# Optimization experiments

Measured on AMD Instinct MI355X. Metric: run time of the kernel, lower is better.

Reference implementation:

```python
import jax, jax.numpy as jnp
import numpy as np

EPS = 1e-5
CHUNK = 512  # chunk of known points for the running-argmin 1-NN search


def nn_idx(unknown, known):
    """1-NN index of each unknown point into known. unknown (B,n,3), known (B,m,3) -> (B,n) int32."""
    B, n, _ = unknown.shape
    m = known.shape[1]
    u2 = jnp.sum(unknown * unknown, axis=-1)  # (B,n)
    # (num_chunks, B, CHUNK, 3)
    kc = known.reshape(B, m // CHUNK, CHUNK, 3).transpose(1, 0, 2, 3)

    def step(carry, kch):
        best_d, best_i, off = carry
        k2 = jnp.sum(kch * kch, axis=-1)  # (B,CHUNK)
        # squared distances for this chunk: (B,n,CHUNK)
        d = u2[:, :, None] - 2.0 * jnp.einsum('bnd,bcd->bnc', unknown, kch) + k2[:, None, :]
        dmin = jnp.min(d, axis=-1)
        imin = jnp.argmin(d, axis=-1).astype(jnp.int32) + off
        upd = dmin < best_d
        return (jnp.where(upd, dmin, best_d), jnp.where(upd, imin, best_i), off + CHUNK), None

    init = (jnp.full((B, n), jnp.inf, unknown.dtype),
            jnp.zeros((B, n), jnp.int32),
            jnp.int32(0))
    (_, best_i, _), _ = jax.lax.scan(step, init, kc)
    return best_i


def bn_relu(x, gamma, beta):
    """Training-mode BatchNorm over (B, n) per channel followed by ReLU. x: (B,C,n)."""
    mean = jnp.mean(x, axis=(0, 2), keepdims=True)
    var = jnp.mean(jnp.square(x - mean), axis=(0, 2), keepdims=True)  # biased, as torch BN
    y = (x - mean) * jax.lax.rsqrt(var + EPS)
    return jax.nn.relu(y * gamma[None, :, None] + beta[None, :, None])


def setup_inputs() -> dict:
    key = jax.random.key(0)
    ks = jax.random.split(key, 8)
    B, n, m, C1, C2 = 2, 65536, 16384, 128, 256
    mlp = [C2 + C1, 256, 128]
    return {
        'unknown': jax.random.normal(ks[0], (B, n, 3), jnp.float32),
        'known': jax.random.normal(ks[1], (B, m, 3), jnp.float32),
        'unknow_feats': jax.random.normal(ks[2], (B, C1, n), jnp.float32),
        'known_feats': jax.random.normal(ks[3], (B, C2, m), jnp.float32),
        'w1': jax.random.normal(ks[4], (mlp[1], mlp[0]), jnp.float32) * (1.0 / np.sqrt(mlp[0])),
        'gamma1': jnp.ones((mlp[1],), jnp.float32),
        'beta1': jnp.zeros((mlp[1],), jnp.float32),
        'w2': jax.random.normal(ks[5], (mlp[2], mlp[1]), jnp.float32) * (1.0 / np.sqrt(mlp[1])),
        'gamma2': jnp.ones((mlp[2],), jnp.float32),
        'beta2': jnp.zeros((mlp[2],), jnp.float32),
    }


def reference(unknown, known, unknow_feats, known_feats, w1, gamma1, beta1, w2, gamma2, beta2):
    idx = nn_idx(unknown, known)  # (B,n) int32
    # gather: (B,C2,m) indexed along m -> (B,C2,n)
    interpolated = jnp.take_along_axis(known_feats, idx[:, None, :], axis=2)
    new_features = jnp.concatenate([interpolated, unknow_feats], axis=1)  # (B,C1+C2,n)
    h = bn_relu(jnp.einsum('oc,bcn->bon', w1, new_features), gamma1, beta1)
    out = bn_relu(jnp.einsum('oc,bcn->bon', w2, h), gamma2, beta2)
    return out  # (B, mlp[-1], n)
```

## Files before the change

### kernel.cpp

```cpp
#include <hip/hip_runtime.h>

typedef unsigned short u16;
typedef unsigned int u32;
typedef __bf16 bf16x8 __attribute__((ext_vector_type(8)));
typedef _Float16 f16;
typedef _Float16 f16x8 __attribute__((ext_vector_type(8)));
typedef float f32x4 __attribute__((ext_vector_type(4)));
typedef float f32x16 __attribute__((ext_vector_type(16)));

#define B_ 2
#define N_ 65536
#define M_ 16384
#define C1_ 128
#define C2_ 256
#define K1_ 384
#define O1_ 256
#define O2_ 128
#define JT_ 512
#define HT_ (JT_/2)
#define EPS2_ 6.0e-3f
#define TFIN_ 1.25e-4f

__device__ __forceinline__ u16 f2bf(float f) {
    u32 u = __float_as_uint(f);
    u32 r = (u + 0x7FFFu + ((u >> 16) & 1u)) >> 16;
    return (u16)r;
}
__device__ __forceinline__ float bf2f(u16 h) {
    return __uint_as_float(((u32)h) << 16);
}
__device__ __forceinline__ u32 pack2(float lo, float hi) {
    return (u32)f2bf(lo) | ((u32)f2bf(hi) << 16);
}
__device__ __forceinline__ uint4 pack8(float4 a, float4 b) {
    uint4 r;
    r.x = pack2(a.x, a.y); r.y = pack2(a.z, a.w);
    r.z = pack2(b.x, b.y); r.w = pack2(b.z, b.w);
    return r;
}
__device__ __forceinline__ u16 h2u(f16 h) {
    union { f16 h; u16 u; } c; c.h = h; return c.u;
}

__device__ __forceinline__ float mul_rn(float a, float b) {
    float p = __fmul_rn(a, b);
    asm volatile("" : "+v"(p));
    return p;
}
__device__ __forceinline__ float sq3_np(float x, float y, float z) {
    return __fadd_rn(__fadd_rn(mul_rn(x, x), mul_rn(y, y)), mul_rn(z, z));
}
__device__ __forceinline__ float dot3_fma(float a0, float b0, float a1, float b1,
                                          float a2, float b2) {
    return fmaf(a2, b2, fmaf(a1, b1, mul_rn(a0, b0)));
}


__global__ __launch_bounds__(256) void k_prep_u(const float* __restrict__ unk,
                                                u16* __restrict__ Aprep) {
    int g = blockIdx.x * 256 + threadIdx.x;
    const float* up = unk + (size_t)g * 3;
    float tx = -2.f * up[0], ty = -2.f * up[1], tz = -2.f * up[2];
    f16 xh = (f16)tx; f16 xl = (f16)(tx - (float)xh);
    f16 yh = (f16)ty; f16 yl = (f16)(ty - (float)yh);
    f16 zh = (f16)tz; f16 zl = (f16)(tz - (float)zh);
    u16 lo[8] = {h2u(xh), h2u(xh), h2u(xl), h2u(yh), h2u(yh), h2u(yl), h2u(zh), h2u(zh)};
    u16 hi[8] = {h2u(zl), 0x3C00u, 0x3C00u, 0, 0, 0, 0, 0};
    u16* tb = Aprep + ((size_t)(g >> 5)) * 512;
    int r = g & 31;
    *(uint4*)(tb + r * 8) = *(uint4*)lo;
    *(uint4*)(tb + (r + 32) * 8) = *(uint4*)hi;
}

__global__ __launch_bounds__(256) void k_prep_k(const float* __restrict__ kn,
                                                u16* __restrict__ Bprep,
                                                float4* __restrict__ kco) {
    int g = blockIdx.x * 256 + threadIdx.x;
    const float* kp = kn + (size_t)g * 3;
    float x = kp[0], y = kp[1], z = kp[2];
    float qv = sq3_np(x, y, z);
    f16 xh = (f16)x; f16 xl = (f16)(x - (float)xh);
    f16 yh = (f16)y; f16 yl = (f16)(y - (float)yh);
    f16 zh = (f16)z; f16 zl = (f16)(z - (float)zh);
    f16 qh = (f16)qv; f16 ql = (f16)(qv - (float)qh);
    u16 lo[8] = {h2u(xh), h2u(xl), h2u(xh), h2u(yh), h2u(yl), h2u(yh), h2u(zh), h2u(zl)};
    u16 hi[8] = {h2u(zh), h2u(qh), h2u(ql), 0x3C00u, 0x3C00u, 0, 0, 0};
    u16* tb = Bprep + ((size_t)(g >> 5)) * 512;
    int r = g & 31;
    *(uint4*)(tb + r * 8) = *(uint4*)lo;
    *(uint4*)(tb + (r + 32) * 8) = *(uint4*)hi;
    kco[g] = make_float4(x, y, z, qv);
}

__global__ __launch_bounds__(256, 4) void k_nn(
        const u16* __restrict__ Aprep, const u16* __restrict__ Bprep,
        const float* __restrict__ unk, const float4* __restrict__ kco,
        unsigned long long* __restrict__ pc) {
    __shared__ unsigned long long cand[256];
    __shared__ float thrS[256];
    const int t = threadIdx.x;
    const int half = blockIdx.y, b = blockIdx.z;
    const int lane = t & 63, w = t >> 6;
    const int rowbase = blockIdx.x * 256;
    const u16* at = Aprep + (((size_t)(b * N_ + rowbase + w * 64)) >> 5) * 512;
    f16x8 af0 = *(const f16x8*)(at + lane * 8);
    f16x8 af1 = *(const f16x8*)(at + 512 + lane * 8);
    const u16* Bp = Bprep + ((size_t)b * JT_ + (size_t)half * HT_) * 512 + lane * 8;
    cand[t] = ~0ULL;

    const f32x16 zz = {0.f,0.f,0.f,0.f,0.f,0.f,0.f,0.f,0.f,0.f,0.f,0.f,0.f,0.f,0.f,0.f};

    f32x16 rm0, rm1;
#pragma unroll
    for (int r = 0; r < 16; ++r) { rm0[r] = 3.4e38f; rm1[r] = 3.4e38f; }

    f16x8 c0 = *(const f16x8*)Bp;
    f16x8 c1 = *(const f16x8*)(Bp + 512);
    for (int tp = 0; tp < HT_; tp += 2) {
        f16x8 n0 = *(const f16x8*)(Bp + 1024);
        f16x8 n1 = *(const f16x8*)(Bp + 1536);
        Bp += 1024;
        f32x16 a  = __builtin_amdgcn_mfma_f32_32x32x16_f16(af0, c0, zz, 0, 0, 0);
        f32x16 ca = __builtin_amdgcn_mfma_f32_32x32x16_f16(af0, c1, zz, 0, 0, 0);
#pragma unroll
        for (int r = 0; r < 16; ++r)
            rm0[r] = fminf(fminf(rm0[r], a[r]), ca[r]);
        a  = __builtin_amdgcn_mfma_f32_32x32x16_f16(af1, c0, zz, 0, 0, 0);
        ca = __builtin_amdgcn_mfma_f32_32x32x16_f16(af1, c1, zz, 0, 0, 0);
#pragma unroll
        for (int r = 0; r < 16; ++r)
            rm1[r] = fminf(fminf(rm1[r], a[r]), ca[r]);
        c0 = n0; c1 = n1;
    }

#pragma unroll
    for (int r = 0; r < 16; ++r) {
        float v0 = rm0[r], v1 = rm1[r];
        v0 = fminf(v0, __shfl_xor(v0, 1));  v1 = fminf(v1, __shfl_xor(v1, 1));
        v0 = fminf(v0, __shfl_xor(v0, 2));  v1 = fminf(v1, __shfl_xor(v1, 2));
        v0 = fminf(v0, __shfl_xor(v0, 4));  v1 = fminf(v1, __shfl_xor(v1, 4));
        v0 = fminf(v0, __shfl_xor(v0, 8));  v1 = fminf(v1, __shfl_xor(v1, 8));
        v0 = fminf(v0, __shfl_xor(v0, 16)); v1 = fminf(v1, __shfl_xor(v1, 16));
        if ((lane & 31) == 0) {
            int rl = w * 64 + ((lane >> 5) << 2) + (r & 3) + 8 * (r >> 2);
            thrS[rl] = v0 + EPS2_;
            thrS[rl + 32] = v1 + EPS2_;
        }
    }
    if (lane >= 32) {
        float tf0 = thrS[w * 64 + (lane & 31)] + TFIN_;
        f16 h0 = (f16)(-tf0);
        af0[3] = h0; af0[4] = (f16)(-tf0 - (float)h0);
        float tf1 = thrS[w * 64 + 32 + (lane & 31)] + TFIN_;
        f16 h1 = (f16)(-tf1);
        af1[3] = h1; af1[4] = (f16)(-tf1 - (float)h1);
    }

    const float4* kcb = kco + (size_t)b * M_;
    const float* ub = unk + (size_t)b * N_ * 3;
    const int rloc0 = w * 64 + ((lane >> 5) << 2);
    const int jb0 = half * (M_ / 2);

    Bp -= (size_t)HT_ * 512;
    c0 = *(const f16x8*)Bp;
    f16x8 c1b = *(const f16x8*)(Bp + 512);
    for (int tt = 0; tt < HT_; ++tt) {
        f16x8 nx = *(const f16x8*)(Bp + 1024);
        Bp += 512;
        f32x16 a0 = __builtin_amdgcn_mfma_f32_32x32x16_f16(af0, c0, zz, 0, 0, 0);
        f32x16 a1 = __builtin_amdgcn_mfma_f32_32x32x16_f16(af1, c0, zz, 0, 0, 0);
        u32 o = 0;
#pragma unroll
        for (int r = 0; r < 16; ++r)
            o |= __float_as_uint(a0[r]) | __float_as_uint(a1[r]);
        if (__ballot((int)o < 0)) {
            int j = jb0 + tt * 32 + (lane & 31);
            float4 kc = kcb[j];
#pragma unroll
            for (int r = 0; r < 16; ++r) {
                if (a0[r] <= 0.f) {
                    int rl = rloc0 + (r & 3) + 8 * (r >> 2);
                    const float* up = ub + (size_t)(rowbase + rl) * 3;
                    float x = up[0], y = up[1], zc = up[2];
                    float uq = sq3_np(x, y, zc);
                    float dot = dot3_fma(x, kc.x, y, kc.y, zc, kc.z);
                    float d = __fadd_rn(fmaf(-2.0f, dot, uq), kc.w);
                    u32 db = __float_as_uint(d);
                    db = (db & 0x80000000u) ? ~db : (db | 0x80000000u);
                    atomicMin(&cand[rl], ((unsigned long long)db << 32) | (u32)j);
                }
                if (a1[r] <= 0.f) {
                    int rl = rloc0 + 32 + (r & 3) + 8 * (r >> 2);
                    const float* up = ub + (size_t)(rowbase + rl) * 3;
                    float x = up[0], y = up[1], zc = up[2];
                    float uq = sq3_np(x, y, zc);
                    float dot = dot3_fma(x, kc.x, y, kc.y, zc, kc.z);
                    float d = __fadd_rn(fmaf(-2.0f, dot, uq), kc.w);
                    u32 db = __float_as_uint(d);
                    db = (db & 0x80000000u) ? ~db : (db | 0x80000000u);
                    atomicMin(&cand[rl], ((unsigned long long)db << 32) | (u32)j);
                }
            }
        }
        c0 = c1b; c1b = nx;
    }
    pc[((size_t)(half * B_ + b)) * N_ + rowbase + t] = cand[t];
}

__global__ __launch_bounds__(256) void k_nn_merge(
        const unsigned long long* __restrict__ pc, int* __restrict__ idx) {
    int g = blockIdx.x * 256 + threadIdx.x;
    unsigned long long a = pc[g];
    unsigned long long c = pc[(size_t)(B_ * N_) + g];
    idx[g] = (int)(u32)((c < a ? c : a) & 0xFFFFFFFFu);
}

__global__ __launch_bounds__(256) void k_tr_kf(const float* __restrict__ kf,
                                               u16* __restrict__ kfT) {
    __shared__ float lt[64][65];
    const int t = threadIdx.x, b = blockIdx.z;
    const int j0 = blockIdx.x * 64, c0 = blockIdx.y * 64;
    const int jl = t & 63, cl4 = t >> 6;
#pragma unroll
    for (int p = 0; p < 16; ++p) {
        int c = c0 + cl4 + p * 4;
        lt[cl4 + p * 4][jl] = kf[((size_t)(b * C2_ + c)) * M_ + j0 + jl];
    }
    __syncthreads();
    const int cl = t & 63, jr4 = t >> 6;
#pragma unroll
    for (int p = 0; p < 16; ++p) {
        int j = j0 + jr4 + p * 4;
        kfT[((size_t)(b * M_ + j)) * C2_ + c0 + cl] = f2bf(lt[cl][jr4 + p * 4]);
    }
}

__global__ __launch_bounds__(256) void k_tr_uf(const float* __restrict__ uf,
                                               u16* __restrict__ newF) {
    __shared__ float lt[64][65];
    const int t = threadIdx.x, b = blockIdx.z;
    const int i0 = blockIdx.x * 64, c0 = blockIdx.y * 64;
    const int il = t & 63, cl4 = t >> 6;
#pragma unroll
    for (int p = 0; p < 16; ++p) {
        int c = c0 + cl4 + p * 4;
        lt[cl4 + p * 4][il] = uf[((size_t)(b * C1_ + c)) * N_ + i0 + il];
    }
    __syncthreads();
    const int cl = t & 63, ir4 = t >> 6;
#pragma unroll
    for (int p = 0; p < 16; ++p) {
        int i = i0 + ir4 + p * 4;
        newF[((size_t)(b * N_ + i)) * K1_ + C2_ + c0 + cl] = f2bf(lt[cl][ir4 + p * 4]);
    }
}

__global__ __launch_bounds__(256) void k_gather(const u16* __restrict__ kfT,
                                                const int* __restrict__ idx,
                                                u16* __restrict__ newF) {
    const int t = threadIdx.x, b = blockIdx.y;
    const int il = t >> 5, qq = t & 31;
    const int i = blockIdx.x * 8 + il;
    const int j = idx[b * N_ + i];
    const uint4* src = (const uint4*)(kfT + ((size_t)(b * M_ + j)) * C2_) + qq;
    uint4* dst = (uint4*)(newF + ((size_t)(b * N_ + i)) * K1_) + qq;
    *dst = *src;
}

__global__ __launch_bounds__(256) void k_gemm1(const u16* __restrict__ newF,
                                               const float* __restrict__ w1,
                                               u16* __restrict__ y1) {
    __shared__ u16 As[128 * 40];
    __shared__ u16 Bs[128 * 40];
    const int t = threadIdx.x, b = blockIdx.z;
    const int i0 = blockIdx.x * 128, o0 = blockIdx.y * 128;
    const int lane = t & 63, wv = t >> 6, wr = wv >> 1, wc = wv & 1;
    const int col = lane & 15, q = lane >> 4;

    const int rA0 = t >> 2, sA0 = t & 3;
    const u16* aS0 = newF + ((size_t)(b * N_ + i0 + rA0)) * K1_ + sA0 * 8;
    const u16* aS1 = aS0 + (size_t)64 * K1_;
    const float* bS0 = w1 + (size_t)(o0 + rA0) * K1_ + sA0 * 8;
    const float* bS1 = bS0 + (size_t)64 * K1_;
    u16* aD0 = &As[rA0 * 40 + sA0 * 8];
    u16* aD1 = aD0 + 64 * 40;
    u16* bD0 = &Bs[rA0 * 40 + sA0 * 8];
    u16* bD1 = bD0 + 64 * 40;

    f32x4 acc[4][4];
#pragma unroll
    for (int m = 0; m < 4; ++m)
#pragma unroll
        for (int n = 0; n < 4; ++n) acc[m][n] = (f32x4){0.f, 0.f, 0.f, 0.f};

    uint4 a0 = *(const uint4*)aS0, a1 = *(const uint4*)aS1;
    float4 f00 = *(const float4*)bS0, f01 = *(const float4*)(bS0 + 4);
    float4 f10 = *(const float4*)bS1, f11 = *(const float4*)(bS1 + 4);

    for (int ks = 0; ks < 12; ++ks) {
        __syncthreads();
        *(uint4*)aD0 = a0; *(uint4*)aD1 = a1;
        *(uint4*)bD0 = pack8(f00, f01); *(uint4*)bD1 = pack8(f10, f11);
        __syncthreads();
        if (ks < 11) {
            int ko = (ks + 1) * 32;
            a0 = *(const uint4*)(aS0 + ko); a1 = *(const uint4*)(aS1 + ko);
            f00 = *(const float4*)(bS0 + ko); f01 = *(const float4*)(bS0 + ko + 4);
            f10 = *(const float4*)(bS1 + ko); f11 = *(const float4*)(bS1 + ko + 4);
        }
        const u16* ap = &As[(wr * 64 + col) * 40 + q * 8];
        const u16* bp = &Bs[(wc * 64 + col) * 40 + q * 8];
        bf16x8 af[4], bfr[4];
#pragma unroll
        for (int m = 0; m < 4; ++m) af[m] = *(const bf16x8*)(ap + m * 640);
#pragma unroll
        for (int n = 0; n < 4; ++n) bfr[n] = *(const bf16x8*)(bp + n * 640);
#pragma unroll
        for (int m = 0; m < 4; ++m)
#pragma unroll
            for (int n = 0; n < 4; ++n)
                acc[m][n] = __builtin_amdgcn_mfma_f32_16x16x32_bf16(af[m], bfr[n], acc[m][n], 0, 0, 0);
    }
#pragma unroll
    for (int m = 0; m < 4; ++m)
#pragma unroll
        for (int n = 0; n < 4; ++n) {
            int go = o0 + wc * 64 + n * 16 + col;
#pragma unroll
            for (int r = 0; r < 4; ++r) {
                int gi = i0 + wr * 64 + m * 16 + q * 4 + r;
                y1[((size_t)(b * N_ + gi)) * O1_ + go] = f2bf(acc[m][n][r]);
            }
        }
}

__global__ __launch_bounds__(256) void k_stats_bf16(const u16* __restrict__ y1,
                                                    float* __restrict__ sum,
                                                    float* __restrict__ sq) {
    const int t = threadIdx.x;
    const int row0 = blockIdx.x * 1024;
    float s = 0.f, qq = 0.f;
    for (int r = 0; r < 1024; ++r) {
        float v = bf2f(y1[((size_t)(row0 + r)) * O1_ + t]);
        s += v; qq = fmaf(v, v, qq);
    }
    atomicAdd(&sum[t], s);
    atomicAdd(&sq[t], qq);
}

__global__ __launch_bounds__(256) void k_stats_f32(const float* __restrict__ y2,
                                                   float* __restrict__ sum,
                                                   float* __restrict__ sq) {
    const int t = threadIdx.x;
    const int o = t & 127, h = t >> 7;
    const int row0 = blockIdx.x * 1024;
    float s = 0.f, qq = 0.f;
    for (int r = 0; r < 512; ++r) {
        float v = y2[((size_t)(row0 + r * 2 + h)) * O2_ + o];
        s += v; qq = fmaf(v, v, qq);
    }
    atomicAdd(&sum[o], s);
    atomicAdd(&sq[o], qq);
}

__global__ void k_bn_fin(const float* __restrict__ sum, const float* __restrict__ sq,
                         const float* __restrict__ gamma, const float* __restrict__ beta,
                         float* __restrict__ scale, float* __restrict__ bias,
                         int C, float invN) {
    int t = threadIdx.x;
    if (t < C) {
        float mean = sum[t] * invN;
        float var = sq[t] * invN - mean * mean;
        float rs = rsqrtf(var + 1e-5f);
        float sc = gamma[t] * rs;
        scale[t] = sc;
        bias[t] = beta[t] - mean * sc;
    }
}

__global__ __launch_bounds__(256) void k_gemm2(const u16* __restrict__ y1,
                                               const float* __restrict__ w2,
                                               const float* __restrict__ s1,
                                               const float* __restrict__ b1,
                                               float* __restrict__ y2) {
    __shared__ u16 As[128 * 40];
    __shared__ u16 Bs[128 * 40];
    const int t = threadIdx.x, b = blockIdx.z;
    const int i0 = blockIdx.x * 128;
    const int lane = t & 63, wv = t >> 6, wr = wv >> 1, wc = wv & 1;
    const int col = lane & 15, q = lane >> 4;

    const int rA0 = t >> 2, sA0 = t & 3;
    const u16* aS0 = y1 + ((size_t)(b * N_ + i0 + rA0)) * O1_ + sA0 * 8;
    const u16* aS1 = aS0 + (size_t)64 * O1_;
    const float* bS0 = w2 + (size_t)rA0 * O1_ + sA0 * 8;
    const float* bS1 = bS0 + (size_t)64 * O1_;
    u16* aD0 = &As[rA0 * 40 + sA0 * 8];
    u16* aD1 = aD0 + 64 * 40;
    u16* bD0 = &Bs[rA0 * 40 + sA0 * 8];
    u16* bD1 = bD0 + 64 * 40;

    f32x4 acc[4][4];
#pragma unroll
    for (int m = 0; m < 4; ++m)
#pragma unroll
        for (int n = 0; n < 4; ++n) acc[m][n] = (f32x4){0.f, 0.f, 0.f, 0.f};

    uint4 a0 = *(const uint4*)aS0, a1 = *(const uint4*)aS1;
    float4 f00 = *(const float4*)bS0, f01 = *(const float4*)(bS0 + 4);
    float4 f10 = *(const float4*)bS1, f11 = *(const float4*)(bS1 + 4);

    for (int ks = 0; ks < 8; ++ks) {
        int oc = ks * 32 + sA0 * 8;
        float4 sc0 = *(const float4*)(s1 + oc), sc1 = *(const float4*)(s1 + oc + 4);
        float4 bb0 = *(const float4*)(b1 + oc), bb1 = *(const float4*)(b1 + oc + 4);
        uint4 h0, h1;
        {
            const u16* hs = (const u16*)&a0;
            float v[8];
            v[0] = fmaxf(fmaf(bf2f(hs[0]), sc0.x, bb0.x), 0.f);
            v[1] = fmaxf(fmaf(bf2f(hs[1]), sc0.y, bb0.y), 0.f);
            v[2] = fmaxf(fmaf(bf2f(hs[2]), sc0.z, bb0.z), 0.f);
            v[3] = fmaxf(fmaf(bf2f(hs[3]), sc0.w, bb0.w), 0.f);
            v[4] = fmaxf(fmaf(bf2f(hs[4]), sc1.x, bb1.x), 0.f);
            v[5] = fmaxf(fmaf(bf2f(hs[5]), sc1.y, bb1.y), 0.f);
            v[6] = fmaxf(fmaf(bf2f(hs[6]), sc1.z, bb1.z), 0.f);
            v[7] = fmaxf(fmaf(bf2f(hs[7]), sc1.w, bb1.w), 0.f);
            h0.x = pack2(v[0], v[1]); h0.y = pack2(v[2], v[3]);
            h0.z = pack2(v[4], v[5]); h0.w = pack2(v[6], v[7]);
        }
        {
            const u16* hs = (const u16*)&a1;
            float v[8];
            v[0] = fmaxf(fmaf(bf2f(hs[0]), sc0.x, bb0.x), 0.f);
            v[1] = fmaxf(fmaf(bf2f(hs[1]), sc0.y, bb0.y), 0.f);
            v[2] = fmaxf(fmaf(bf2f(hs[2]), sc0.z, bb0.z), 0.f);
            v[3] = fmaxf(fmaf(bf2f(hs[3]), sc0.w, bb0.w), 0.f);
            v[4] = fmaxf(fmaf(bf2f(hs[4]), sc1.x, bb1.x), 0.f);
            v[5] = fmaxf(fmaf(bf2f(hs[5]), sc1.y, bb1.y), 0.f);
            v[6] = fmaxf(fmaf(bf2f(hs[6]), sc1.z, bb1.z), 0.f);
            v[7] = fmaxf(fmaf(bf2f(hs[7]), sc1.w, bb1.w), 0.f);
            h1.x = pack2(v[0], v[1]); h1.y = pack2(v[2], v[3]);
            h1.z = pack2(v[4], v[5]); h1.w = pack2(v[6], v[7]);
        }
        __syncthreads();
        *(uint4*)aD0 = h0; *(uint4*)aD1 = h1;
        *(uint4*)bD0 = pack8(f00, f01); *(uint4*)bD1 = pack8(f10, f11);
        __syncthreads();
        if (ks < 7) {
            int ko = (ks + 1) * 32;
            a0 = *(const uint4*)(aS0 + ko); a1 = *(const uint4*)(aS1 + ko);
            f00 = *(const float4*)(bS0 + ko); f01 = *(const float4*)(bS0 + ko + 4);
            f10 = *(const float4*)(bS1 + ko); f11 = *(const float4*)(bS1 + ko + 4);
        }
        const u16* ap = &As[(wr * 64 + col) * 40 + q * 8];
        const u16* bp = &Bs[(wc * 64 + col) * 40 + q * 8];
        bf16x8 af[4], bfr[4];
#pragma unroll
        for (int m = 0; m < 4; ++m) af[m] = *(const bf16x8*)(ap + m * 640);
#pragma unroll
        for (int n = 0; n < 4; ++n) bfr[n] = *(const bf16x8*)(bp + n * 640);
#pragma unroll
        for (int m = 0; m < 4; ++m)
#pragma unroll
            for (int n = 0; n < 4; ++n)
                acc[m][n] = __builtin_amdgcn_mfma_f32_16x16x32_bf16(af[m], bfr[n], acc[m][n], 0, 0, 0);
    }
#pragma unroll
    for (int m = 0; m < 4; ++m)
#pragma unroll
        for (int n = 0; n < 4; ++n) {
            int go = wc * 64 + n * 16 + col;
#pragma unroll
            for (int r = 0; r < 4; ++r) {
                int gi = i0 + wr * 64 + m * 16 + q * 4 + r;
                y2[((size_t)(b * N_ + gi)) * O2_ + go] = acc[m][n][r];
            }
        }
}

__global__ __launch_bounds__(256) void k_out(const float* __restrict__ y2,
                                             const float* __restrict__ s2,
                                             const float* __restrict__ b2,
                                             float* __restrict__ out) {
    __shared__ float lt[64 * 65];
    const int t = threadIdx.x, b = blockIdx.z;
    const int i0 = blockIdx.x * 64, o0 = blockIdx.y * 64;
    const int oc = t & 63, ir4 = t >> 6;
    const float sc = s2[o0 + oc], bs = b2[o0 + oc];
#pragma unroll
    for (int p = 0; p < 16; ++p) {
        int i = i0 + ir4 + p * 4;
        float v = y2[((size_t)(b * N_ + i)) * O2_ + o0 + oc];
        lt[oc * 65 + ir4 + p * 4] = fmaxf(fmaf(v, sc, bs), 0.f);
    }
    __syncthreads();
    const int il = t & 63, or4 = t >> 6;
#pragma unroll
    for (int p = 0; p < 16; ++p) {
        int o = o0 + or4 + p * 4;
        out[((size_t)(b * O2_ + o)) * N_ + i0 + il] = lt[(or4 + p * 4) * 65 + il];
    }
}

extern "C" void kernel_launch(void* const* d_in, const int* in_sizes, int n_in,
                              void* d_out, int out_size, void* d_ws, size_t ws_size,
                              hipStream_t stream) {
    const float* unknown = (const float*)d_in[0];
    const float* known   = (const float*)d_in[1];
    const float* uf      = (const float*)d_in[2];
    const float* kf      = (const float*)d_in[3];
    const float* w1      = (const float*)d_in[4];
    const float* g1      = (const float*)d_in[5];
    const float* be1     = (const float*)d_in[6];
    const float* w2      = (const float*)d_in[7];
    const float* g2      = (const float*)d_in[8];
    const float* be2     = (const float*)d_in[9];
    float* out = (float*)d_out;

    char* w = (char*)d_ws;
    float* bn1_sum = (float*)w;
    float* bn1_sq  = bn1_sum + 256;
    float* bn2_sum = bn1_sq + 256;
    float* bn2_sq  = bn2_sum + 128;
    float* s1 = (float*)(w + 4096);
    float* b1 = s1 + 256;
    float* s2 = b1 + 256;
    float* b2 = s2 + 128;
    int* idx = (int*)(w + 8192);
    u16* newF = (u16*)(w + 532480);
    float* y2 = (float*)(w + 532480);
    size_t R2 = 532480 + 100663296ULL;
    u16*   Aprep = (u16*)(w + R2);
    u16*   Bprep = (u16*)(w + R2 + 4194304ULL);
    float4* kco  = (float4*)(w + R2 + 5242880ULL);
    unsigned long long* pc = (unsigned long long*)(w + R2 + 5767168ULL);
    u16*  kfT = (u16*)(w + R2 + 16777216ULL);
    u16*   y1 = (u16*)(w + R2);

    hipMemsetAsync(w, 0, 3072, stream);

    k_prep_u<<<512, 256, 0, stream>>>(unknown, Aprep);
    k_prep_k<<<128, 256, 0, stream>>>(known, Bprep, kco);
    k_nn<<<dim3(N_ / 256, 2, B_), 256, 0, stream>>>(Aprep, Bprep, unknown, kco, pc);
    k_nn_merge<<<512, 256, 0, stream>>>(pc, idx);
    k_tr_kf<<<dim3(256, 4, 2), 256, 0, stream>>>(kf, kfT);
    k_tr_uf<<<dim3(1024, 2, 2), 256, 0, stream>>>(uf, newF);
    k_gather<<<dim3(8192, 2), 256, 0, stream>>>(kfT, idx, newF);
    k_gemm1<<<dim3(512, 2, 2), 256, 0, stream>>>(newF, w1, y1);
    k_stats_bf16<<<128, 256, 0, stream>>>(y1, bn1_sum, bn1_sq);
    k_bn_fin<<<1, 256, 0, stream>>>(bn1_sum, bn1_sq, g1, be1, s1, b1, 256, 1.f / 131072.f);
    k_gemm2<<<dim3(512, 1, 2), 256, 0, stream>>>(y1, w2, s1, b1, y2);
    k_stats_f32<<<128, 256, 0, stream>>>(y2, bn2_sum, bn2_sq);
    k_bn_fin<<<1, 256, 0, stream>>>(bn2_sum, bn2_sq, g2, be2, s2, b2, 128, 1.f / 131072.f);
    k_out<<<dim3(1024, 2, 2), 256, 0, stream>>>(y2, s2, b2, out);
}
```

Before: 582.2 us.

## Fuse BN statistics into GEMM epilogues, rescale NN filter, add group-level refine skip

The BatchNorm sum and sum-of-squares reductions move into the epilogues of both GEMM kernels, using wave shuffles and atomics, so the two separate stats kernels and their full re-reads of y1 and y2 are dropped. The fp16 MFMA distance filter in the NN kernel is rescaled by 256 to use more of fp16's range, with the candidate threshold constants scaled to match. The filter-hit test now uses per-group mins with __any, so refinement runs only for row groups that actually have candidates. Risks: atomic float accumulation order changes the BN statistics slightly, and the rescaled fp16 thresholds could change which candidates pass the filter.

```diff
diff --git a/kernel.cpp b/kernel.cpp
--- a/kernel.cpp
+++ b/kernel.cpp
@@ -18,8 +18,8 @@
 #define O2_ 128
 #define JT_ 512
 #define HT_ (JT_/2)
-#define EPS2_ 6.0e-3f
-#define TFIN_ 1.25e-4f
+#define EPS2_ 131.072f
+#define TFIN_ 8.0f
 
 __device__ __forceinline__ u16 f2bf(float f) {
     u32 u = __float_as_uint(f);
@@ -60,12 +60,12 @@
                                                 u16* __restrict__ Aprep) {
     int g = blockIdx.x * 256 + threadIdx.x;
     const float* up = unk + (size_t)g * 3;
-    float tx = -2.f * up[0], ty = -2.f * up[1], tz = -2.f * up[2];
+    float tx = -512.f * up[0], ty = -512.f * up[1], tz = -512.f * up[2];
     f16 xh = (f16)tx; f16 xl = (f16)(tx - (float)xh);
     f16 yh = (f16)ty; f16 yl = (f16)(ty - (float)yh);
     f16 zh = (f16)tz; f16 zl = (f16)(tz - (float)zh);
     u16 lo[8] = {h2u(xh), h2u(xh), h2u(xl), h2u(yh), h2u(yh), h2u(yl), h2u(zh), h2u(zh)};
-    u16 hi[8] = {h2u(zl), 0x3C00u, 0x3C00u, 0, 0, 0, 0, 0};
+    u16 hi[8] = {h2u(zl), 0x5C00u, 0x5C00u, 0, 0, 0, 0, 0};
     u16* tb = Aprep + ((size_t)(g >> 5)) * 512;
     int r = g & 31;
     *(uint4*)(tb + r * 8) = *(uint4*)lo;
@@ -79,12 +79,13 @@
     const float* kp = kn + (size_t)g * 3;
     float x = kp[0], y = kp[1], z = kp[2];
     float qv = sq3_np(x, y, z);
-    f16 xh = (f16)x; f16 xl = (f16)(x - (float)xh);
-    f16 yh = (f16)y; f16 yl = (f16)(y - (float)yh);
-    f16 zh = (f16)z; f16 zl = (f16)(z - (float)zh);
-    f16 qh = (f16)qv; f16 ql = (f16)(qv - (float)qh);
+    float sx = 256.f * x, sy = 256.f * y, sz = 256.f * z, sq = 256.f * qv;
+    f16 xh = (f16)sx; f16 xl = (f16)(sx - (float)xh);
+    f16 yh = (f16)sy; f16 yl = (f16)(sy - (float)yh);
+    f16 zh = (f16)sz; f16 zl = (f16)(sz - (float)zh);
+    f16 qh = (f16)sq; f16 ql = (f16)(sq - (float)qh);
     u16 lo[8] = {h2u(xh), h2u(xl), h2u(xh), h2u(yh), h2u(yl), h2u(yh), h2u(zh), h2u(zl)};
-    u16 hi[8] = {h2u(zh), h2u(qh), h2u(ql), 0x3C00u, 0x3C00u, 0, 0, 0};
+    u16 hi[8] = {h2u(zh), h2u(qh), h2u(ql), 0x5C00u, 0x5C00u, 0, 0, 0};
     u16* tb = Bprep + ((size_t)(g >> 5)) * 512;
     int r = g & 31;
     *(uint4*)(tb + r * 8) = *(uint4*)lo;
@@ -148,10 +149,10 @@
         }
     }
     if (lane >= 32) {
-        float tf0 = thrS[w * 64 + (lane & 31)] + TFIN_;
+        float tf0 = (thrS[w * 64 + (lane & 31)] + TFIN_) * 0.00390625f;
         f16 h0 = (f16)(-tf0);
         af0[3] = h0; af0[4] = (f16)(-tf0 - (float)h0);
-        float tf1 = thrS[w * 64 + 32 + (lane & 31)] + TFIN_;
+        float tf1 = (thrS[w * 64 + 32 + (lane & 31)] + TFIN_) * 0.00390625f;
         f16 h1 = (f16)(-tf1);
         af1[3] = h1; af1[4] = (f16)(-tf1 - (float)h1);
     }
@@ -160,6 +161,19 @@
     const float* ub = unk + (size_t)b * N_ * 3;
     const int rloc0 = w * 64 + ((lane >> 5) << 2);
     const int jb0 = half * (M_ / 2);
+
+#define REFINE(RL, AV)                                                         \
+    if ((AV) <= 0.f) {                                                         \
+        int rl = (RL);                                                         \
+        const float* up = ub + (size_t)(rowbase + rl) * 3;                     \
+        float x = up[0], y = up[1], zc = up[2];                                \
+        float uq = sq3_np(x, y, zc);                                           \
+        float dot = dot3_fma(x, kc.x, y, kc.y, zc, kc.z);                      \
+        float d = __fadd_rn(fmaf(-2.0f, dot, uq), kc.w);                       \
+        u32 db = __float_as_uint(d);                                           \
+        db = (db & 0x80000000u) ? ~db : (db | 0x80000000u);                    \
+        atomicMin(&cand[rl], ((unsigned long long)db << 32) | (u32)j);         \
+    }
 
     Bp -= (size_t)HT_ * 512;
     c0 = *(const f16x8*)Bp;
@@ -169,41 +183,34 @@
         Bp += 512;
         f32x16 a0 = __builtin_amdgcn_mfma_f32_32x32x16_f16(af0, c0, zz, 0, 0, 0);
         f32x16 a1 = __builtin_amdgcn_mfma_f32_32x32x16_f16(af1, c0, zz, 0, 0, 0);
-        u32 o = 0;
-#pragma unroll
-        for (int r = 0; r < 16; ++r)
-            o |= __float_as_uint(a0[r]) | __float_as_uint(a1[r]);
-        if (__ballot((int)o < 0)) {
+        float gm0[4], gm1[4];
+#pragma unroll
+        for (int g = 0; g < 4; ++g) {
+            gm0[g] = fminf(fminf(a0[4*g], a0[4*g+1]), fminf(a0[4*g+2], a0[4*g+3]));
+            gm1[g] = fminf(fminf(a1[4*g], a1[4*g+1]), fminf(a1[4*g+2], a1[4*g+3]));
+        }
+        float gall = fminf(fminf(fminf(gm0[0], gm0[1]), fminf(gm0[2], gm0[3])),
+                           fminf(fminf(gm1[0], gm1[1]), fminf(gm1[2], gm1[3])));
+        if (__ballot(gall <= 0.f)) {
             int j = jb0 + tt * 32 + (lane & 31);
             float4 kc = kcb[j];
 #pragma unroll
-            for (int r = 0; r < 16; ++r) {
-                if (a0[r] <= 0.f) {
-                    int rl = rloc0 + (r & 3) + 8 * (r >> 2);
-                    const float* up = ub + (size_t)(rowbase + rl) * 3;
-                    float x = up[0], y = up[1], zc = up[2];
-                    float uq = sq3_np(x, y, zc);
-                    float dot = dot3_fma(x, kc.x, y, kc.y, zc, kc.z);
-                    float d = __fadd_rn(fmaf(-2.0f, dot, uq), kc.w);
-                    u32 db = __float_as_uint(d);
-                    db = (db & 0x80000000u) ? ~db : (db | 0x80000000u);
-                    atomicMin(&cand[rl], ((unsigned long long)db << 32) | (u32)j);
+            for (int g = 0; g < 4; ++g) {
+                if (__any(gm0[g] <= 0.f)) {
+#pragma unroll
+                    for (int rr = 0; rr < 4; ++rr)
+                        REFINE(rloc0 + 8 * g + rr, a0[4*g+rr])
                 }
-                if (a1[r] <= 0.f) {
-                    int rl = rloc0 + 32 + (r & 3) + 8 * (r >> 2);
-                    const float* up = ub + (size_t)(rowbase + rl) * 3;
-                    float x = up[0], y = up[1], zc = up[2];
-                    float uq = sq3_np(x, y, zc);
-                    float dot = dot3_fma(x, kc.x, y, kc.y, zc, kc.z);
-                    float d = __fadd_rn(fmaf(-2.0f, dot, uq), kc.w);
-                    u32 db = __float_as_uint(d);
-                    db = (db & 0x80000000u) ? ~db : (db | 0x80000000u);
-                    atomicMin(&cand[rl], ((unsigned long long)db << 32) | (u32)j);
+                if (__any(gm1[g] <= 0.f)) {
+#pragma unroll
+                    for (int rr = 0; rr < 4; ++rr)
+                        REFINE(rloc0 + 32 + 8 * g + rr, a1[4*g+rr])
                 }
             }
         }
         c0 = c1b; c1b = nx;
     }
+#undef REFINE
     pc[((size_t)(half * B_ + b)) * N_ + rowbase + t] = cand[t];
 }
 
@@ -269,7 +276,9 @@
 
 __global__ __launch_bounds__(256) void k_gemm1(const u16* __restrict__ newF,
                                                const float* __restrict__ w1,
-                                               u16* __restrict__ y1) {
+                                               u16* __restrict__ y1,
+                                               float* __restrict__ bsum,
+                                               float* __restrict__ bsq) {
     __shared__ u16 As[128 * 40];
     __shared__ u16 Bs[128 * 40];
     const int t = threadIdx.x, b = blockIdx.z;
@@ -321,6 +330,9 @@
             for (int n = 0; n < 4; ++n)
                 acc[m][n] = __builtin_amdgcn_mfma_f32_16x16x32_bf16(af[m], bfr[n], acc[m][n], 0, 0, 0);
     }
+    float ssum[4], ssq[4];
+#pragma unroll
+    for (int n = 0; n < 4; ++n) { ssum[n] = 0.f; ssq[n] = 0.f; }
 #pragma unroll
     for (int m = 0; m < 4; ++m)
 #pragma unroll
@@ -329,38 +341,23 @@
 #pragma unroll
             for (int r = 0; r < 4; ++r) {
                 int gi = i0 + wr * 64 + m * 16 + q * 4 + r;
-                y1[((size_t)(b * N_ + gi)) * O1_ + go] = f2bf(acc[m][n][r]);
+                u16 hv = f2bf(acc[m][n][r]);
+                y1[((size_t)(b * N_ + gi)) * O1_ + go] = hv;
+                float v = bf2f(hv);
+                ssum[n] += v; ssq[n] = fmaf(v, v, ssq[n]);
             }
         }
-}
-
-__global__ __launch_bounds__(256) void k_stats_bf16(const u16* __restrict__ y1,
-                                                    float* __restrict__ sum,
-                                                    float* __restrict__ sq) {
-    const int t = threadIdx.x;
-    const int row0 = blockIdx.x * 1024;
-    float s = 0.f, qq = 0.f;
-    for (int r = 0; r < 1024; ++r) {
-        float v = bf2f(y1[((size_t)(row0 + r)) * O1_ + t]);
-        s += v; qq = fmaf(v, v, qq);
-    }
-    atomicAdd(&sum[t], s);
-    atomicAdd(&sq[t], qq);
-}
-
-__global__ __launch_bounds__(256) void k_stats_f32(const float* __restrict__ y2,
-                                                   float* __restrict__ sum,
-                                                   float* __restrict__ sq) {
-    const int t = threadIdx.x;
-    const int o = t & 127, h = t >> 7;
-    const int row0 = blockIdx.x * 1024;
-    float s = 0.f, qq = 0.f;
-    for (int r = 0; r < 512; ++r) {
-        float v = y2[((size_t)(row0 + r * 2 + h)) * O2_ + o];
-        s += v; qq = fmaf(v, v, qq);
-    }
-    atomicAdd(&sum[o], s);
-    atomicAdd(&sq[o], qq);
+#pragma unroll
+    for (int n = 0; n < 4; ++n) {
+        float s = ssum[n], qv = ssq[n];
+        s += __shfl_xor(s, 16); qv += __shfl_xor(qv, 16);
+        s += __shfl_xor(s, 32); qv += __shfl_xor(qv, 32);
+        if (q == 0) {
+            int go = o0 + wc * 64 + n * 16 + col;
+            atomicAdd(&bsum[go], s);
+            atomicAdd(&bsq[go], qv);
+        }
+    }
 }
 
 __global__ void k_bn_fin(const float* __restrict__ sum, const float* __restrict__ sq,
@@ -382,7 +379,9 @@
                                                const float* __restrict__ w2,
                                                const float* __restrict__ s1,
                                                const float* __restrict__ b1,
-                                               float* __restrict__ y2) {
+                                               float* __restrict__ y2,
+                                               float* __restrict__ bsum,
+                                               float* __restrict__ bsq) {
     __shared__ u16 As[128 * 40];
     __shared__ u16 Bs[128 * 40];
     const int t = threadIdx.x, b = blockIdx.z;
@@ -466,6 +465,9 @@
             for (int n = 0; n < 4; ++n)
                 acc[m][n] = __builtin_amdgcn_mfma_f32_16x16x32_bf16(af[m], bfr[n], acc[m][n], 0, 0, 0);
     }
+    float ssum[4], ssq[4];
+#pragma unroll
+    for (int n = 0; n < 4; ++n) { ssum[n] = 0.f; ssq[n] = 0.f; }
 #pragma unroll
     for (int m = 0; m < 4; ++m)
 #pragma unroll
@@ -474,9 +476,22 @@
 #pragma unroll
             for (int r = 0; r < 4; ++r) {
                 int gi = i0 + wr * 64 + m * 16 + q * 4 + r;
-                y2[((size_t)(b * N_ + gi)) * O2_ + go] = acc[m][n][r];
+                float v = acc[m][n][r];
+                y2[((size_t)(b * N_ + gi)) * O2_ + go] = v;
+                ssum[n] += v; ssq[n] = fmaf(v, v, ssq[n]);
             }
         }
+#pragma unroll
+    for (int n = 0; n < 4; ++n) {
+        float s = ssum[n], qv = ssq[n];
+        s += __shfl_xor(s, 16); qv += __shfl_xor(qv, 16);
+        s += __shfl_xor(s, 32); qv += __shfl_xor(qv, 32);
+        if (q == 0) {
+            int go = wc * 64 + n * 16 + col;
+            atomicAdd(&bsum[go], s);
+            atomicAdd(&bsq[go], qv);
+        }
+    }
 }
 
 __global__ __launch_bounds__(256) void k_out(const float* __restrict__ y2,
@@ -547,11 +562,9 @@
     k_tr_kf<<<dim3(256, 4, 2), 256, 0, stream>>>(kf, kfT);
     k_tr_uf<<<dim3(1024, 2, 2), 256, 0, stream>>>(uf, newF);
     k_gather<<<dim3(8192, 2), 256, 0, stream>>>(kfT, idx, newF);
-    k_gemm1<<<dim3(512, 2, 2), 256, 0, stream>>>(newF, w1, y1);
-    k_stats_bf16<<<128, 256, 0, stream>>>(y1, bn1_sum, bn1_sq);
+    k_gemm1<<<dim3(512, 2, 2), 256, 0, stream>>>(newF, w1, y1, bn1_sum, bn1_sq);
     k_bn_fin<<<1, 256, 0, stream>>>(bn1_sum, bn1_sq, g1, be1, s1, b1, 256, 1.f / 131072.f);
-    k_gemm2<<<dim3(512, 1, 2), 256, 0, stream>>>(y1, w2, s1, b1, y2);
-    k_stats_f32<<<128, 256, 0, stream>>>(y2, bn2_sum, bn2_sq);
+    k_gemm2<<<dim3(512, 1, 2), 256, 0, stream>>>(y1, w2, s1, b1, y2, bn2_sum, bn2_sq);
     k_bn_fin<<<1, 256, 0, stream>>>(bn2_sum, bn2_sq, g2, be2, s2, b2, 128, 1.f / 131072.f);
     k_out<<<dim3(1024, 2, 2), 256, 0, stream>>>(y2, s2, b2, out);
 }
```

Measured after the change: 592.8 us. No clear change (+1.8%).
